# Kernel optimization log

Measured on AMD Instinct MI355X. Metric: run time of the kernel, lower is better.

The kernel has to match this reference:

```python
import jax, jax.numpy as jnp
from jax import lax
import numpy as np

GB_MAX = 3      # BandEst guard-band upper bound
RB = 1          # refer_band
PAD = RB + 1    # refer_band + init_guard_band(1)
N_OFF = 16      # ring offsets: kernel (4,4) -> N=16
BN_EPS = 1e-5

def _ring_offsets():
    idx = np.arange(-PAD, PAD + 1)
    X, Y = np.meshgrid(idx, idx, indexing='ij')
    hp = wp = 2 * PAD + 1
    def ring(M):
        return np.concatenate([M[0:RB, 0:wp - RB].ravel(), M[0:hp - RB, wp - RB:wp].ravel(),
                               M[hp - RB:hp, RB:wp].ravel(), M[RB:hp, 0:RB].ravel()])
    return ring(X).astype(np.float32), ring(Y).astype(np.float32)

PRF_X, PRF_Y = _ring_offsets()
BLOCK = np.repeat(np.arange(4), N_OFF // 4)  # offset n -> direction block (top,right,bottom,left)


def q_shift(x, H, W, shift=1, gamma=0.25):
    B, T, C = x.shape
    img = x.transpose(0, 2, 1).reshape(B, C, H, W)
    g = int(C * gamma)
    out = jnp.zeros_like(img)
    out = out.at[:, 0:g, :, shift:].set(img[:, 0:g, :, :W - shift])
    out = out.at[:, g:2 * g, :, :W - shift].set(img[:, g:2 * g, :, shift:])
    out = out.at[:, 2 * g:3 * g, shift:, :].set(img[:, 2 * g:3 * g, :H - shift, :])
    out = out.at[:, 3 * g:4 * g, :H - shift, :].set(img[:, 3 * g:4 * g, shift:, :])
    out = out.at[:, 4 * g:].set(img[:, 4 * g:])
    return out.reshape(B, C, T).transpose(0, 2, 1)


def bi_wkv(w, u, k, v):
    # Bi-directional WKV: y_t = (sum_{i<t} e^{-(t-1-i)w + k_i} v_i + e^{u+k_t} v_t
    #                            + sum_{i>t} e^{-(i-1-t)w + k_i} v_i) / (same with v->1)
    B, T, C = k.shape
    kT = k.transpose(1, 0, 2)
    vT = v.transpose(1, 0, 2)

    def step(carry, kv):
        m, a, b = carry  # state represents e^m * (a, b): (sum exp, weighted v)
        kt, vt = kv
        out = (m, a, b)  # exclusive prefix (excludes current token)
        m2 = jnp.maximum(m - w, kt)
        e1 = jnp.exp(m - w - m2)
        e2 = jnp.exp(kt - m2)
        return (m2, e1 * a + e2, e1 * b + e2 * vt), out

    init = (jnp.full((B, C), -1e38, k.dtype), jnp.zeros((B, C), k.dtype), jnp.zeros((B, C), k.dtype))
    _, (mf, af, bf) = lax.scan(step, init, (kT, vT))
    _, (mb, ab, bb) = lax.scan(step, init, (kT[::-1], vT[::-1]))
    mb, ab, bb = mb[::-1], ab[::-1], bb[::-1]
    ms = u + kT
    M = jnp.maximum(jnp.maximum(mf, mb), ms)
    ef, eb, es = jnp.exp(mf - M), jnp.exp(mb - M), jnp.exp(ms - M)
    num = ef * bf + eb * bb + es * vT
    den = ef * af + eb * ab + es
    return (num / den).transpose(1, 0, 2)


def band_est(x, cvw, cvb, bns_v, bnb_v, chw, chb, bns_h, bnb_h):
    dn = ('NCHW', 'OIHW', 'NCHW')
    gv = lax.conv_general_dilated(x, cvw, (1, 1), ((GB_MAX, GB_MAX), (0, 0)), dimension_numbers=dn) + cvb[None, :, None, None]
    gh = lax.conv_general_dilated(x, chw, (1, 1), ((0, 0), (GB_MAX, GB_MAX)), dimension_numbers=dn) + chb[None, :, None, None]
    inv = np.float32(1.0 / np.sqrt(1.0 + BN_EPS))  # eval BN: running mean 0, var 1
    gv = gv * (bns_v * inv)[None, :, None, None] + bnb_v[None, :, None, None]
    gh = gh * (bns_h * inv)[None, :, None, None] + bnb_h[None, :, None, None]
    return jnp.concatenate([jax.nn.sigmoid(gv), jax.nn.sigmoid(gh)], 1) * (GB_MAX - 1)


def _gather(xp_flat, ix, iy, wp, h, w):
    b, c = xp_flat.shape[0], xp_flat.shape[1]
    idx = (ix * wp + iy).reshape(b, 1, -1)
    return jnp.take_along_axis(xp_flat, idx, axis=2).reshape(b, c, h, w, N_OFF)


def ada_peak(x_img, cvw, cvb, bns_v, bnb_v, chw, chb, bns_h, bnb_h):
    b, c, h, w = x_img.shape
    xp = jnp.pad(x_img, ((0, 0), (0, 0), (PAD, PAD), (PAD, PAD)), mode='edge')
    hp, wp = h + 2 * PAD, w + 2 * PAD
    xp_flat = xp.reshape(b, c, hp * wp)
    gb = band_est(x_img, cvw, cvb, bns_v, bnb_v, chw, chb, bns_h, bnb_h)  # (b,4,h,w)
    zero = jnp.zeros_like(gb[:, 0])
    mvx = jnp.stack([-gb[:, 0], zero, gb[:, 1], zero], -1)  # (b,h,w,4) per block
    mvy = jnp.stack([zero, gb[:, 3], zero, -gb[:, 2]], -1)
    move_x = mvx[..., BLOCK]  # (b,h,w,16)
    move_y = mvy[..., BLOCK]
    cx = jnp.arange(PAD, h + PAD, dtype=x_img.dtype)
    cy = jnp.arange(PAD, w + PAD, dtype=x_img.dtype)
    px = cx[None, :, None, None] + jnp.asarray(PRF_X)[None, None, None, :] + move_x
    py = cy[None, None, :, None] + jnp.asarray(PRF_Y)[None, None, None, :] + move_y
    flx = jnp.floor(lax.stop_gradient(px))
    fly = jnp.floor(lax.stop_gradient(py))
    q_lt_x = jnp.clip(flx, 0, hp - 1)
    q_lt_y = jnp.clip(fly, 0, wp - 1)
    q_rb_x = jnp.clip(flx + 1, 0, hp - 1)
    q_rb_y = jnp.clip(fly + 1, 0, wp - 1)
    pxc = jnp.clip(px, 0, hp - 1)
    pyc = jnp.clip(py, 0, wp - 1)
    g_lt = (1 + (q_lt_x - pxc)) * (1 + (q_lt_y - pyc))
    g_rb = (1 - (q_rb_x - pxc)) * (1 - (q_rb_y - pyc))
    x_lt = _gather(xp_flat, q_lt_x.astype(jnp.int32), q_lt_y.astype(jnp.int32), wp, h, w)
    x_rb = _gather(xp_flat, q_rb_x.astype(jnp.int32), q_rb_y.astype(jnp.int32), wp, h, w)
    x_r = g_lt[:, None] * x_lt + g_rb[:, None] * x_rb
    return x_img[..., None] - x_r  # (b,c,h,w,N): center-minus-reference peak feature


def setup_inputs():
    key = jax.random.key(0)
    B, H, W, C = 2, 64, 64, 192
    ks = jax.random.split(key, 16)
    s = 0.02
    return {
        'x': jax.random.normal(ks[0], (B, H * W, C), jnp.float32),
        'h': H, 'w': W,
        'mix_k': jax.random.uniform(ks[1], (1, 1, C), jnp.float32),
        'mix_v': jax.random.uniform(ks[2], (1, 1, C), jnp.float32),
        'mix_r': jax.random.uniform(ks[3], (1, 1, C), jnp.float32),
        'Wk': jax.random.normal(ks[4], (C, C), jnp.float32) * s,
        'Wv': jax.random.normal(ks[5], (C, C), jnp.float32) * s,
        'Wr': jax.random.normal(ks[6], (C, C), jnp.float32) * s,
        'Wo': jax.random.normal(ks[7], (C, C), jnp.float32) * s,
        'spatial_decay': jax.random.normal(ks[8], (C,), jnp.float32),
        'spatial_first': jax.random.normal(ks[9], (C,), jnp.float32),
        'cvw': jax.random.normal(ks[10], (2, C, 2 * GB_MAX + 1, 1), jnp.float32) * s,
        'cvb': jnp.zeros((2,), jnp.float32),
        'bns_v': jnp.ones((2,), jnp.float32),
        'bnb_v': jnp.zeros((2,), jnp.float32),
        'chw': jax.random.normal(ks[11], (2, C, 1, 2 * GB_MAX + 1), jnp.float32) * s,
        'chb': jnp.zeros((2,), jnp.float32),
        'bns_h': jnp.ones((2,), jnp.float32),
        'bnb_h': jnp.zeros((2,), jnp.float32),
    }


def reference(x, h, w, mix_k, mix_v, mix_r, Wk, Wv, Wr, Wo, spatial_decay, spatial_first,
              cvw, cvb, bns_v, bnb_v, chw, chb, bns_h, bnb_h):
    B, T, C = x.shape
    xx = q_shift(x, h, w)
    xk = x * mix_k + xx * (1 - mix_k)
    xv = x * mix_v + xx * (1 - mix_v)
    xr = x * mix_r + xx * (1 - mix_r)
    k = xk @ Wk
    v = xv @ Wv
    sr = jax.nn.sigmoid(xr @ Wr)
    # deformable peak branch (AdaPeak2D) on the token grid, pooled over the N=16 ring samples
    x_img = x.transpose(0, 2, 1).reshape(B, C, h, w)
    peak = ada_peak(x_img, cvw, cvb, bns_v, bnb_v, chw, chb, bns_h, bnb_h).mean(-1)
    v = v + peak.reshape(B, C, T).transpose(0, 2, 1)
    y = bi_wkv(spatial_decay / T, spatial_first / T, k, v)
    return (sr * y) @ Wo
```

## Files before the change

### kernel.cpp

```cpp
#include <hip/hip_runtime.h>
#include <hip/hip_bf16.h>

#define BATCH 2
#define TLEN 4096
#define CC 192
#define NTOT 576
#define PADC 2

__device__ __constant__ float PRF_X[16] = {-2,-2,-2,-2, -2,-1,0,1, 2,2,2,2, -1,0,1,2};
__device__ __constant__ float PRF_Y[16] = {-2,-1,0,1, 2,2,2,2, -1,0,1,2, -2,-2,-2,-2};

#define ASWZ(n) ((n) + (((n) >> 5) << 2))

__global__ __launch_bounds__(256) void k_build_wcat(const float* __restrict__ Wk,
                                                    const float* __restrict__ Wv,
                                                    const float* __restrict__ Wr,
                                                    const float* __restrict__ mk,
                                                    const float* __restrict__ mv,
                                                    const float* __restrict__ mr,
                                                    float* __restrict__ Wcat) {
    int idx = blockIdx.x * 256 + threadIdx.x;
    if (idx >= 384 * NTOT) return;
    int r   = idx / NTOT;
    int col = idx - r * NTOT;
    int cb = col / CC;
    int cc = col - cb * CC;
    const float* W   = (cb == 0) ? Wk : (cb == 1) ? Wv : Wr;
    const float* mix = (cb == 0) ? mk : (cb == 1) ? mv : mr;
    float v;
    if (r < CC) v = mix[r] * W[r * CC + cc];
    else        v = (1.0f - mix[r - CC]) * W[(r - CC) * CC + cc];
    Wcat[idx] = v;
}

__global__ __launch_bounds__(256) void k_gemm1(const float* __restrict__ x,
                                               const float* __restrict__ Wcat,
                                               float* __restrict__ ZTk,
                                               float* __restrict__ Zv,
                                               float* __restrict__ ZTr) {
    __shared__ float As[2][16][140];
    __shared__ float Bs[2][16][68];
    const int tid = threadIdx.x;
    const int bm = blockIdx.y * 128;
    const int bn = blockIdx.x * 64;
    const int tx = tid & 15, ty = tid >> 4;
    const int ar  = tid >> 1;
    const int akh = (tid & 1) * 8;
    const int bk  = tid >> 4;
    const int bn4 = (tid & 15) * 4;

    const int row = bm + ar;
    const int t   = row & (TLEN - 1);
    const int ri  = t >> 6, rj = t & 63;

    float acc[8][4] = {};
    float4 a0, a1, b0;

    auto loadG = [&](int k0, float4& ra0, float4& ra1, float4& rb0) {
        if (k0 < CC) {
            const float* pa = x + (size_t)row * CC + k0 + akh;
            ra0 = *(const float4*)pa;
            ra1 = *(const float4*)(pa + 4);
        } else {
            int c = k0 - CC + akh;
            int g = c / 48;
            int dr; bool ok;
            if      (g == 0) { dr = -1;  ok = (rj > 0);  }
            else if (g == 1) { dr =  1;  ok = (rj < 63); }
            else if (g == 2) { dr = -64; ok = (ri > 0);  }
            else             { dr =  64; ok = (ri < 63); }
            if (ok) {
                const float* pa = x + (size_t)(row + dr) * CC + c;
                ra0 = *(const float4*)pa;
                ra1 = *(const float4*)(pa + 4);
            } else {
                ra0 = make_float4(0.f, 0.f, 0.f, 0.f);
                ra1 = make_float4(0.f, 0.f, 0.f, 0.f);
            }
        }
        rb0 = *(const float4*)(Wcat + (size_t)(k0 + bk) * NTOT + bn + bn4);
    };
    auto stage = [&](int buf, float4 ra0, float4 ra1, float4 rb0) {
        int sa = ASWZ(ar);
        As[buf][akh + 0][sa] = ra0.x; As[buf][akh + 1][sa] = ra0.y;
        As[buf][akh + 2][sa] = ra0.z; As[buf][akh + 3][sa] = ra0.w;
        As[buf][akh + 4][sa] = ra1.x; As[buf][akh + 5][sa] = ra1.y;
        As[buf][akh + 6][sa] = ra1.z; As[buf][akh + 7][sa] = ra1.w;
        *(float4*)&Bs[buf][bk][bn4] = rb0;
    };

    loadG(0, a0, a1, b0);
    stage(0, a0, a1, b0);
    __syncthreads();

    const int abase = ASWZ(ty * 8);
    int buf = 0;
    for (int it = 0; it < 24; ++it) {
        if (it < 23) loadG((it + 1) * 16, a0, a1, b0);
#pragma unroll
        for (int kk = 0; kk < 16; ++kk) {
            float av[8], bv[4];
            *(float4*)&av[0] = *(const float4*)&As[buf][kk][abase];
            *(float4*)&av[4] = *(const float4*)&As[buf][kk][abase + 4];
            *(float4*)&bv[0] = *(const float4*)&Bs[buf][kk][tx * 4];
#pragma unroll
            for (int ii = 0; ii < 8; ++ii)
#pragma unroll
                for (int jj = 0; jj < 4; ++jj)
                    acc[ii][jj] = fmaf(av[ii], bv[jj], acc[ii][jj]);
        }
        if (it < 23) {
            stage(buf ^ 1, a0, a1, b0);
            __syncthreads();
            buf ^= 1;
        }
    }

    const int sec = bn / CC;
    const int col0 = bn - sec * CC + tx * 4;
    if (sec == 1) {
#pragma unroll
        for (int ii = 0; ii < 8; ++ii) {
            int r2 = bm + ty * 8 + ii;
            float4 o = {acc[ii][0], acc[ii][1], acc[ii][2], acc[ii][3]};
            *(float4*)(Zv + (size_t)r2 * CC + col0) = o;
        }
    } else {
        float* D = (sec == 0) ? ZTk : ZTr;
        int row0 = bm + ty * 8;
#pragma unroll
        for (int jj = 0; jj < 4; ++jj) {
            float4 o0 = {acc[0][jj], acc[1][jj], acc[2][jj], acc[3][jj]};
            float4 o1 = {acc[4][jj], acc[5][jj], acc[6][jj], acc[7][jj]};
            float* p = D + (size_t)(col0 + jj) * 8192 + row0;
            *(float4*)p = o0;
            *(float4*)(p + 4) = o1;
        }
    }
}

__global__ __launch_bounds__(256) void k_gemm2(const float* __restrict__ AT,
                                               const float* __restrict__ B,
                                               float* __restrict__ Cmat) {
    __shared__ float As[2][16][132];
    __shared__ float Bs[2][16][68];
    const int tid = threadIdx.x;
    const int bm = blockIdx.y * 128;
    const int bn = blockIdx.x * 64;
    const int tx = tid & 15, ty = tid >> 4;
    const int ak  = tid >> 4;
    const int am8 = (tid & 15) * 8;
    const int bkr = tid >> 4;
    const int bn4 = (tid & 15) * 4;

    float acc[8][4] = {};
    float4 a0, a1, b0;

    auto loadG = [&](int k0, float4& ra0, float4& ra1, float4& rb0) {
        const float* pa = AT + (size_t)(k0 + ak) * 8192 + bm + am8;
        ra0 = *(const float4*)pa;
        ra1 = *(const float4*)(pa + 4);
        rb0 = *(const float4*)(B + (size_t)(k0 + bkr) * CC + bn + bn4);
    };
    auto stage = [&](int buf, float4 ra0, float4 ra1, float4 rb0) {
        *(float4*)&As[buf][ak][am8]     = ra0;
        *(float4*)&As[buf][ak][am8 + 4] = ra1;
        *(float4*)&Bs[buf][bkr][bn4]    = rb0;
    };

    loadG(0, a0, a1, b0);
    stage(0, a0, a1, b0);
    __syncthreads();

    int buf = 0;
    for (int it = 0; it < 12; ++it) {
        if (it < 11) loadG((it + 1) * 16, a0, a1, b0);
#pragma unroll
        for (int kk = 0; kk < 16; ++kk) {
            float av[8], bv[4];
            *(float4*)&av[0] = *(const float4*)&As[buf][kk][ty * 8];
            *(float4*)&av[4] = *(const float4*)&As[buf][kk][ty * 8 + 4];
            *(float4*)&bv[0] = *(const float4*)&Bs[buf][kk][tx * 4];
#pragma unroll
            for (int ii = 0; ii < 8; ++ii)
#pragma unroll
                for (int jj = 0; jj < 4; ++jj)
                    acc[ii][jj] = fmaf(av[ii], bv[jj], acc[ii][jj]);
        }
        if (it < 11) {
            stage(buf ^ 1, a0, a1, b0);
            __syncthreads();
            buf ^= 1;
        }
    }
#pragma unroll
    for (int ii = 0; ii < 8; ++ii) {
        int row = bm + ty * 8 + ii;
        float4 o0 = {acc[ii][0], acc[ii][1], acc[ii][2], acc[ii][3]};
        *(float4*)(Cmat + (size_t)row * CC + bn + tx * 4) = o0;
    }
}

__global__ __launch_bounds__(192) void k_bandpeak(const float* __restrict__ x,
                                                  const float* __restrict__ cvw,
                                                  const float* __restrict__ cvb,
                                                  const float* __restrict__ bns_v,
                                                  const float* __restrict__ bnb_v,
                                                  const float* __restrict__ chw,
                                                  const float* __restrict__ chb,
                                                  const float* __restrict__ bns_h,
                                                  const float* __restrict__ bnb_h,
                                                  float* __restrict__ Zv) {
    int pixg = blockIdx.x;
    int b   = pixg >> 12;
    int pix = pixg & 4095;
    int i = pix >> 6, j = pix & 63;
    int c = threadIdx.x;
    size_t xbase = (size_t)b * TLEN * CC;

    float sv0 = 0.f, sv1 = 0.f, sh0 = 0.f, sh1 = 0.f;
#pragma unroll
    for (int t = 0; t < 7; ++t) {
        int ii = i + t - 3;
        if (ii >= 0 && ii < 64) {
            float xv = x[xbase + (size_t)(ii * 64 + j) * CC + c];
            sv0 = fmaf(xv, cvw[(0 * CC + c) * 7 + t], sv0);
            sv1 = fmaf(xv, cvw[(1 * CC + c) * 7 + t], sv1);
        }
        int jj = j + t - 3;
        if (jj >= 0 && jj < 64) {
            float xh = x[xbase + (size_t)(i * 64 + jj) * CC + c];
            sh0 = fmaf(xh, chw[(0 * CC + c) * 7 + t], sh0);
            sh1 = fmaf(xh, chw[(1 * CC + c) * 7 + t], sh1);
        }
    }
    __shared__ float red[4][CC];
    __shared__ float gsh[4];
    red[0][c] = sv0; red[1][c] = sv1; red[2][c] = sh0; red[3][c] = sh1;
    __syncthreads();
    if (c < 64) {
#pragma unroll
        for (int r = 0; r < 4; ++r) {
            float v = red[r][c] + red[r][c + 64] + red[r][c + 128];
            v += __shfl_xor(v, 32);
            v += __shfl_xor(v, 16);
            v += __shfl_xor(v, 8);
            v += __shfl_xor(v, 4);
            v += __shfl_xor(v, 2);
            v += __shfl_xor(v, 1);
            if (c == 0) {
                const float inv = 0.9999950000374997f;
                float bias, sc, sh;
                if (r < 2) { bias = cvb[r];     sc = bns_v[r];     sh = bnb_v[r]; }
                else       { bias = chb[r - 2]; sc = bns_h[r - 2]; sh = bnb_h[r - 2]; }
                float g = (v + bias) * (sc * inv) + sh;
                gsh[r] = 2.0f / (1.0f + expf(-g));
            }
        }
    }
    __syncthreads();

    __shared__ int   l_lt[16], l_rb[16];
    __shared__ float l_glt[16], l_grb[16];
    if (c < 16) {
        int n = c, blk = n >> 2;
        float mx = (blk == 0) ? -gsh[0] : (blk == 2) ? gsh[1] : 0.0f;
        float my = (blk == 1) ?  gsh[3] : (blk == 3) ? -gsh[2] : 0.0f;
        float px = (float)(i + PADC) + PRF_X[n] + mx;
        float py = (float)(j + PADC) + PRF_Y[n] + my;
        float flx = floorf(px), fly = floorf(py);
        float qltx = fminf(fmaxf(flx, 0.f), 67.f);
        float qlty = fminf(fmaxf(fly, 0.f), 67.f);
        float qrbx = fminf(fmaxf(flx + 1.f, 0.f), 67.f);
        float qrby = fminf(fmaxf(fly + 1.f, 0.f), 67.f);
        float pxc = fminf(fmaxf(px, 0.f), 67.f);
        float pyc = fminf(fmaxf(py, 0.f), 67.f);
        float glt = (1.f + (qltx - pxc)) * (1.f + (qlty - pyc));
        float grb = (1.f - (qrbx - pxc)) * (1.f - (qrby - pyc));
        int sltx = min(max((int)qltx - PADC, 0), 63);
        int slty = min(max((int)qlty - PADC, 0), 63);
        int srbx = min(max((int)qrbx - PADC, 0), 63);
        int srby = min(max((int)qrby - PADC, 0), 63);
        l_lt[n] = sltx * 64 + slty;
        l_rb[n] = srbx * 64 + srby;
        l_glt[n] = glt;
        l_grb[n] = grb;
    }
    __syncthreads();

    float acc = 0.f;
#pragma unroll
    for (int n = 0; n < 16; ++n) {
        acc = fmaf(l_glt[n], x[xbase + (size_t)l_lt[n] * CC + c], acc);
        acc = fmaf(l_grb[n], x[xbase + (size_t)l_rb[n] * CC + c], acc);
    }
    float peak = x[xbase + (size_t)pix * CC + c] - acc * 0.0625f;
    Zv[((size_t)b * TLEN + pix) * CC + c] += peak;
}

__global__ __launch_bounds__(256) void k_transv(const float* __restrict__ Zv,
                                                float* __restrict__ ZTv) {
    __shared__ float tile[64][65];
    int tid = threadIdx.x;
    int rb = (blockIdx.x & 127) * 64;
    int cb = (blockIdx.x >> 7) * 64;
    int tr  = tid >> 4;
    int tc4 = (tid & 15) * 4;
#pragma unroll
    for (int q = 0; q < 4; ++q) {
        int r = tr + q * 16;
        float4 v = *(const float4*)(Zv + (size_t)(rb + r) * CC + cb + tc4);
        *(float4*)&tile[r][tc4] = v;
    }
    __syncthreads();
#pragma unroll
    for (int q = 0; q < 4; ++q) {
        int ccol = tr + q * 16;
        float4 o = {tile[tc4 + 0][ccol], tile[tc4 + 1][ccol],
                    tile[tc4 + 2][ccol], tile[tc4 + 3][ccol]};
        *(float4*)(ZTv + (size_t)(cb + ccol) * 8192 + rb + tc4) = o;
    }
}

__global__ __launch_bounds__(256) void k_wkv2(const float* __restrict__ ZT,
                                              float* __restrict__ PT,
                                              const float* __restrict__ sd,
                                              const float* __restrict__ sf) {
    const int NTH = 256, CH = 16;
    int c = blockIdx.x % CC;
    int b = blockIdx.x / CC;
    const float w = sd[c] * (1.0f / 4096.0f);
    const float u = sf[c] * (1.0f / 4096.0f);

    __shared__ float s_m[NTH], s_a[NTH], s_b[NTH], s_L[NTH];

    int tid = threadIdx.x;
    int s = tid * CH;
    size_t rowbase = (size_t)b * TLEN;

    float kr[CH], vr[CH], rr[CH];
    {
        const float* pk = ZT + (size_t)c * 8192 + rowbase + s;
        const float* pv = ZT + (size_t)(CC + c) * 8192 + rowbase + s;
        const float* pr = ZT + (size_t)(2 * CC + c) * 8192 + rowbase + s;
#pragma unroll
        for (int q = 0; q < 4; ++q) {
            *(float4*)&kr[q * 4] = *(const float4*)(pk + q * 4);
            *(float4*)&vr[q * 4] = *(const float4*)(pv + q * 4);
            *(float4*)&rr[q * 4] = *(const float4*)(pr + q * 4);
        }
    }

    float m = -1e38f, a = 0.f, bb = 0.f;
#pragma unroll
    for (int jj = 0; jj < CH; ++jj) {
        float kt = kr[jj], vt = vr[jj];
        float m2 = fmaxf(m - w, kt);
        float e1 = expf(m - w - m2);
        float e2 = expf(kt - m2);
        a = e1 * a + e2;
        bb = e1 * bb + e2 * vt;
        m = m2;
    }
    s_m[tid] = m; s_a[tid] = a; s_b[tid] = bb; s_L[tid] = (float)CH;
    float L = (float)CH;
    for (int d = 1; d < NTH; d <<= 1) {
        __syncthreads();
        float pm = 0, pa = 0, pb = 0, pL = 0;
        bool has = (tid >= d);
        if (has) { pm = s_m[tid - d]; pa = s_a[tid - d]; pb = s_b[tid - d]; pL = s_L[tid - d]; }
        __syncthreads();
        if (has) {
            float pdec = pm - L * w;
            float m2 = fmaxf(pdec, m);
            float e1 = expf(pdec - m2);
            float e2 = expf(m - m2);
            a  = e1 * pa + e2 * a;
            bb = e1 * pb + e2 * bb;
            m = m2; L += pL;
            s_m[tid] = m; s_a[tid] = a; s_b[tid] = bb; s_L[tid] = L;
        }
    }
    __syncthreads();
    float fm = -1e38f, fa = 0.f, fb = 0.f;
    if (tid > 0) { fm = s_m[tid - 1]; fa = s_a[tid - 1]; fb = s_b[tid - 1]; }
    __syncthreads();

    m = -1e38f; a = 0.f; bb = 0.f;
#pragma unroll
    for (int jj = CH - 1; jj >= 0; --jj) {
        float kt = kr[jj], vt = vr[jj];
        float m2 = fmaxf(m - w, kt);
        float e1 = expf(m - w - m2);
        float e2 = expf(kt - m2);
        a = e1 * a + e2;
        bb = e1 * bb + e2 * vt;
        m = m2;
    }
    s_m[tid] = m; s_a[tid] = a; s_b[tid] = bb; s_L[tid] = (float)CH;
    L = (float)CH;
    for (int d = 1; d < NTH; d <<= 1) {
        __syncthreads();
        float pm = 0, pa = 0, pb = 0, pL = 0;
        bool has = (tid + d) < NTH;
        if (has) { pm = s_m[tid + d]; pa = s_a[tid + d]; pb = s_b[tid + d]; pL = s_L[tid + d]; }
        __syncthreads();
        if (has) {
            float pdec = pm - L * w;
            float m2 = fmaxf(m, pdec);
            float e1 = expf(m - m2);
            float e2 = expf(pdec - m2);
            a  = e1 * a + e2 * pa;
            bb = e1 * bb + e2 * pb;
            m = m2; L += pL;
            s_m[tid] = m; s_a[tid] = a; s_b[tid] = bb; s_L[tid] = L;
        }
    }
    __syncthreads();
    float bm = -1e38f, ba = 0.f, bbv = 0.f;
    if (tid < NTH - 1) { bm = s_m[tid + 1]; ba = s_a[tid + 1]; bbv = s_b[tid + 1]; }

    float em[CH], ea[CH], eb[CH];
    m = bm; a = ba; bb = bbv;
#pragma unroll
    for (int jj = CH - 1; jj >= 0; --jj) {
        em[jj] = m; ea[jj] = a; eb[jj] = bb;
        float kt = kr[jj], vt = vr[jj];
        float m2 = fmaxf(m - w, kt);
        float e1 = expf(m - w - m2);
        float e2 = expf(kt - m2);
        a = e1 * a + e2;
        bb = e1 * bb + e2 * vt;
        m = m2;
    }

    m = fm; a = fa; bb = fb;
#pragma unroll
    for (int jj = 0; jj < CH; ++jj) {
        float kt = kr[jj], vt = vr[jj];
        float ms = u + kt;
        float M = fmaxf(fmaxf(m, em[jj]), ms);
        float ef  = expf(m - M);
        float ebk = expf(em[jj] - M);
        float es  = expf(ms - M);
        float num = ef * bb + ebk * eb[jj] + es * vt;
        float den = ef * a + ebk * ea[jj] + es;
        float y = num / den;
        float sr = 1.0f / (1.0f + expf(-rr[jj]));
        PT[(size_t)c * 8192 + rowbase + s + jj] = sr * y;
        float m2 = fmaxf(m - w, kt);
        float e1 = expf(m - w - m2);
        float e2 = expf(kt - m2);
        a = e1 * a + e2;
        bb = e1 * bb + e2 * vt;
        m = m2;
    }
}

extern "C" void kernel_launch(void* const* d_in, const int* in_sizes, int n_in,
                              void* d_out, int out_size, void* d_ws, size_t ws_size,
                              hipStream_t stream) {
    const float* x     = (const float*)d_in[0];
    const float* mix_k = (const float*)d_in[3];
    const float* mix_v = (const float*)d_in[4];
    const float* mix_r = (const float*)d_in[5];
    const float* Wk    = (const float*)d_in[6];
    const float* Wv    = (const float*)d_in[7];
    const float* Wr    = (const float*)d_in[8];
    const float* Wo    = (const float*)d_in[9];
    const float* sd    = (const float*)d_in[10];
    const float* sf    = (const float*)d_in[11];
    const float* cvw   = (const float*)d_in[12];
    const float* cvb   = (const float*)d_in[13];
    const float* bns_v = (const float*)d_in[14];
    const float* bnb_v = (const float*)d_in[15];
    const float* chw   = (const float*)d_in[16];
    const float* chb   = (const float*)d_in[17];
    const float* bns_h = (const float*)d_in[18];
    const float* bnb_h = (const float*)d_in[19];
    float* out = (float*)d_out;
    float* ws  = (float*)d_ws;

    float* Zv   = ws;
    float* ZT   = ws + 1572864;
    float* Wcat = ws + 6291456;
    float* ZTk  = ZT;
    float* ZTv  = ZT + 1572864;
    float* ZTr  = ZT + 3145728;
    float* PT   = Zv;

    k_build_wcat<<<864, 256, 0, stream>>>(Wk, Wv, Wr, mix_k, mix_v, mix_r, Wcat);
    k_gemm1<<<dim3(9, 64), 256, 0, stream>>>(x, Wcat, ZTk, Zv, ZTr);
    k_bandpeak<<<8192, 192, 0, stream>>>(x, cvw, cvb, bns_v, bnb_v, chw, chb, bns_h, bnb_h, Zv);
    k_transv<<<384, 256, 0, stream>>>(Zv, ZTv);
    k_wkv2<<<384, 256, 0, stream>>>(ZT, PT, sd, sf);
    k_gemm2<<<dim3(3, 64), 256, 0, stream>>>(PT, Wo, out);
}
```

Measured before the change: 238.4 us.

## Run both projection GEMMs on bf16 MFMA with split hi/lo precision

Replaces the FP32 FMA tiled GEMMs with MFMA bf16 kernels. Each fp32 operand is split into a high and a low bf16 part, and three MFMA products are summed to keep near-fp32 accuracy. New prep kernels split x, build the transposed mixed weight and Wo matrices, and transpose/split the WKV output into row-major bf16. This adds extra passes and memory traffic for the conversions in exchange for much higher matrix throughput.

```diff
diff --git a/kernel.cpp b/kernel.cpp
--- a/kernel.cpp
+++ b/kernel.cpp
@@ -4,200 +4,289 @@
 #define BATCH 2
 #define TLEN 4096
 #define CC 192
-#define NTOT 576
 #define PADC 2
+
+typedef __attribute__((ext_vector_type(8))) short bf16x8;
+typedef __attribute__((ext_vector_type(4))) float f32x4;
 
 __device__ __constant__ float PRF_X[16] = {-2,-2,-2,-2, -2,-1,0,1, 2,2,2,2, -1,0,1,2};
 __device__ __constant__ float PRF_Y[16] = {-2,-1,0,1, 2,2,2,2, -1,0,1,2, -2,-2,-2,-2};
 
-#define ASWZ(n) ((n) + (((n) >> 5) << 2))
-
-__global__ __launch_bounds__(256) void k_build_wcat(const float* __restrict__ Wk,
-                                                    const float* __restrict__ Wv,
-                                                    const float* __restrict__ Wr,
-                                                    const float* __restrict__ mk,
-                                                    const float* __restrict__ mv,
-                                                    const float* __restrict__ mr,
-                                                    float* __restrict__ Wcat) {
+__device__ __forceinline__ unsigned short f2bf(float f) {
+    unsigned u = __float_as_uint(f);
+    u = (u + 0x7FFF + ((u >> 16) & 1)) >> 16;
+    return (unsigned short)u;
+}
+__device__ __forceinline__ float bf2f(unsigned short h) {
+    return __uint_as_float(((unsigned)h) << 16);
+}
+
+__global__ __launch_bounds__(256) void k_split_x(const float* __restrict__ x,
+                                                 unsigned short* __restrict__ XH,
+                                                 unsigned short* __restrict__ XL,
+                                                 unsigned short* __restrict__ ZP) {
+    if (blockIdx.x == 0 && threadIdx.x < 32) ZP[threadIdx.x] = 0;
     int idx = blockIdx.x * 256 + threadIdx.x;
-    if (idx >= 384 * NTOT) return;
-    int r   = idx / NTOT;
-    int col = idx - r * NTOT;
-    int cb = col / CC;
-    int cc = col - cb * CC;
-    const float* W   = (cb == 0) ? Wk : (cb == 1) ? Wv : Wr;
-    const float* mix = (cb == 0) ? mk : (cb == 1) ? mv : mr;
-    float v;
-    if (r < CC) v = mix[r] * W[r * CC + cc];
-    else        v = (1.0f - mix[r - CC]) * W[(r - CC) * CC + cc];
-    Wcat[idx] = v;
-}
-
-__global__ __launch_bounds__(256) void k_gemm1(const float* __restrict__ x,
-                                               const float* __restrict__ Wcat,
-                                               float* __restrict__ ZTk,
-                                               float* __restrict__ Zv,
-                                               float* __restrict__ ZTr) {
-    __shared__ float As[2][16][140];
-    __shared__ float Bs[2][16][68];
-    const int tid = threadIdx.x;
+    float4 v = *(const float4*)(x + (size_t)idx * 4);
+    ushort4 hh, ll;
+    float f, fh;
+    f = v.x; hh.x = f2bf(f); fh = bf2f(hh.x); ll.x = f2bf(f - fh);
+    f = v.y; hh.y = f2bf(f); fh = bf2f(hh.y); ll.y = f2bf(f - fh);
+    f = v.z; hh.z = f2bf(f); fh = bf2f(hh.z); ll.z = f2bf(f - fh);
+    f = v.w; hh.w = f2bf(f); fh = bf2f(hh.w); ll.w = f2bf(f - fh);
+    *(ushort4*)(XH + (size_t)idx * 4) = hh;
+    *(ushort4*)(XL + (size_t)idx * 4) = ll;
+}
+
+__global__ __launch_bounds__(256) void k_wcat_t(const float* __restrict__ Wk,
+                                                const float* __restrict__ Wv,
+                                                const float* __restrict__ Wr,
+                                                const float* __restrict__ mk,
+                                                const float* __restrict__ mv,
+                                                const float* __restrict__ mr,
+                                                unsigned short* __restrict__ WTH,
+                                                unsigned short* __restrict__ WTL) {
+    int idx = blockIdx.x * 256 + threadIdx.x;
+    int n = idx / 384, k = idx - n * 384;
+    int sec = n / CC, nc = n - sec * CC;
+    const float* W   = (sec == 0) ? Wk : (sec == 1) ? Wv : Wr;
+    const float* mix = (sec == 0) ? mk : (sec == 1) ? mv : mr;
+    float wv = (k < CC) ? mix[k] * W[k * CC + nc]
+                        : (1.0f - mix[k - CC]) * W[(k - CC) * CC + nc];
+    unsigned short h = f2bf(wv);
+    WTH[idx] = h;
+    WTL[idx] = f2bf(wv - bf2f(h));
+}
+
+__global__ __launch_bounds__(256) void k_prep_wo(const float* __restrict__ Wo,
+                                                 unsigned short* __restrict__ WoTH,
+                                                 unsigned short* __restrict__ WoTL) {
+    int idx = blockIdx.x * 256 + threadIdx.x;
+    int n = idx / CC, k = idx - n * CC;
+    float wv = Wo[k * CC + n];
+    unsigned short h = f2bf(wv);
+    WoTH[idx] = h;
+    WoTL[idx] = f2bf(wv - bf2f(h));
+}
+
+__global__ __launch_bounds__(128, 2) void k_gemm1_mfma(
+        const unsigned short* __restrict__ XH, const unsigned short* __restrict__ XL,
+        const unsigned short* __restrict__ WTH, const unsigned short* __restrict__ WTL,
+        const unsigned short* __restrict__ ZP,
+        float* __restrict__ ZTk, float* __restrict__ Zv, float* __restrict__ ZTr) {
+    __shared__ unsigned short sAh[128 * 32], sAl[128 * 32];
+    __shared__ unsigned short sBh[64 * 32],  sBl[64 * 32];
+    const int tid  = threadIdx.x;
+    const int w    = tid >> 6;
+    const int lane = tid & 63;
+    const int bx = blockIdx.x;
     const int bm = blockIdx.y * 128;
+    const int bn = bx * 64;
+
+    const int lc  = tid & 3;
+    const int ar0 = tid >> 2;
+
+    f32x4 acc[4][4];
+#pragma unroll
+    for (int i = 0; i < 4; ++i)
+#pragma unroll
+        for (int j = 0; j < 4; ++j) acc[i][j] = f32x4{0.f, 0.f, 0.f, 0.f};
+
+    uint4 rA[8], rB[4];
+
+    auto loadA = [&](int step) {
+        int k0 = step * 32;
+#pragma unroll
+        for (int q = 0; q < 4; ++q) {
+            int rloc = ar0 + q * 32;
+            int rg = bm + rloc;
+            const unsigned short *srcH, *srcL;
+            if (k0 < CC) {
+                size_t o = (size_t)rg * CC + k0 + lc * 8;
+                srcH = XH + o; srcL = XL + o;
+            } else {
+                int c = k0 - CC + lc * 8;
+                int g = c / 48;
+                int t = rg & (TLEN - 1);
+                int ri = t >> 6, rj = t & 63;
+                int dr; bool ok;
+                if      (g == 0) { dr = -1;  ok = (rj > 0);  }
+                else if (g == 1) { dr =  1;  ok = (rj < 63); }
+                else if (g == 2) { dr = -64; ok = (ri > 0);  }
+                else             { dr =  64; ok = (ri < 63); }
+                if (ok) { size_t o = (size_t)(rg + dr) * CC + c; srcH = XH + o; srcL = XL + o; }
+                else    { srcH = ZP; srcL = ZP; }
+            }
+            rA[q * 2]     = *(const uint4*)srcH;
+            rA[q * 2 + 1] = *(const uint4*)srcL;
+        }
+    };
+    auto loadB = [&](int step) {
+        int k0 = step * 32;
+#pragma unroll
+        for (int q = 0; q < 2; ++q) {
+            int col = ar0 + q * 32;
+            size_t o = (size_t)(bn + col) * 384 + k0 + lc * 8;
+            rB[q * 2]     = *(const uint4*)(WTH + o);
+            rB[q * 2 + 1] = *(const uint4*)(WTL + o);
+        }
+    };
+    auto writeS = [&]() {
+#pragma unroll
+        for (int q = 0; q < 4; ++q) {
+            int off = (ar0 + q * 32) * 32 + lc * 8;
+            *(uint4*)&sAh[off] = rA[q * 2];
+            *(uint4*)&sAl[off] = rA[q * 2 + 1];
+        }
+#pragma unroll
+        for (int q = 0; q < 2; ++q) {
+            int off = (ar0 + q * 32) * 32 + lc * 8;
+            *(uint4*)&sBh[off] = rB[q * 2];
+            *(uint4*)&sBl[off] = rB[q * 2 + 1];
+        }
+    };
+
+    const int r15 = lane & 15, ksub = lane >> 4;
+    const int pc8 = ksub * 8;
+
+    loadA(0); loadB(0);
+    for (int step = 0; step < 12; ++step) {
+        __syncthreads();
+        writeS();
+        __syncthreads();
+        if (step < 11) { loadA(step + 1); loadB(step + 1); }
+        bf16x8 ah[4], al[4], bh[4], bl[4];
+#pragma unroll
+        for (int f = 0; f < 4; ++f) {
+            int ra = (w * 64 + f * 16 + r15) * 32 + pc8;
+            ah[f] = *(const bf16x8*)&sAh[ra];
+            al[f] = *(const bf16x8*)&sAl[ra];
+            int rb = (f * 16 + r15) * 32 + pc8;
+            bh[f] = *(const bf16x8*)&sBh[rb];
+            bl[f] = *(const bf16x8*)&sBl[rb];
+        }
+#pragma unroll
+        for (int fr = 0; fr < 4; ++fr)
+#pragma unroll
+            for (int fc = 0; fc < 4; ++fc) {
+                acc[fr][fc] = __builtin_amdgcn_mfma_f32_16x16x32_bf16(ah[fr], bh[fc], acc[fr][fc], 0, 0, 0);
+                acc[fr][fc] = __builtin_amdgcn_mfma_f32_16x16x32_bf16(ah[fr], bl[fc], acc[fr][fc], 0, 0, 0);
+                acc[fr][fc] = __builtin_amdgcn_mfma_f32_16x16x32_bf16(al[fr], bh[fc], acc[fr][fc], 0, 0, 0);
+            }
+    }
+
+    const int sec   = bx / 3;
+    const int cbase = (bx - sec * 3) * 64;
+#pragma unroll
+    for (int fr = 0; fr < 4; ++fr) {
+        int row0 = bm + w * 64 + fr * 16 + ksub * 4;
+#pragma unroll
+        for (int fc = 0; fc < 4; ++fc) {
+            int col = cbase + fc * 16 + r15;
+            f32x4 v = acc[fr][fc];
+            if (sec == 1) {
+#pragma unroll
+                for (int rg = 0; rg < 4; ++rg)
+                    Zv[(size_t)(row0 + rg) * CC + col] = v[rg];
+            } else {
+                float* D = (sec == 0) ? ZTk : ZTr;
+                *(float4*)(D + (size_t)col * 8192 + row0) = make_float4(v[0], v[1], v[2], v[3]);
+            }
+        }
+    }
+}
+
+__global__ __launch_bounds__(128, 2) void k_gemm2_mfma(
+        const unsigned short* __restrict__ PH, const unsigned short* __restrict__ PL,
+        const unsigned short* __restrict__ WoTH, const unsigned short* __restrict__ WoTL,
+        float* __restrict__ out) {
+    __shared__ unsigned short sAh[128 * 32], sAl[128 * 32];
+    __shared__ unsigned short sBh[64 * 32],  sBl[64 * 32];
+    const int tid  = threadIdx.x;
+    const int w    = tid >> 6;
+    const int lane = tid & 63;
     const int bn = blockIdx.x * 64;
-    const int tx = tid & 15, ty = tid >> 4;
-    const int ar  = tid >> 1;
-    const int akh = (tid & 1) * 8;
-    const int bk  = tid >> 4;
-    const int bn4 = (tid & 15) * 4;
-
-    const int row = bm + ar;
-    const int t   = row & (TLEN - 1);
-    const int ri  = t >> 6, rj = t & 63;
-
-    float acc[8][4] = {};
-    float4 a0, a1, b0;
-
-    auto loadG = [&](int k0, float4& ra0, float4& ra1, float4& rb0) {
-        if (k0 < CC) {
-            const float* pa = x + (size_t)row * CC + k0 + akh;
-            ra0 = *(const float4*)pa;
-            ra1 = *(const float4*)(pa + 4);
-        } else {
-            int c = k0 - CC + akh;
-            int g = c / 48;
-            int dr; bool ok;
-            if      (g == 0) { dr = -1;  ok = (rj > 0);  }
-            else if (g == 1) { dr =  1;  ok = (rj < 63); }
-            else if (g == 2) { dr = -64; ok = (ri > 0);  }
-            else             { dr =  64; ok = (ri < 63); }
-            if (ok) {
-                const float* pa = x + (size_t)(row + dr) * CC + c;
-                ra0 = *(const float4*)pa;
-                ra1 = *(const float4*)(pa + 4);
-            } else {
-                ra0 = make_float4(0.f, 0.f, 0.f, 0.f);
-                ra1 = make_float4(0.f, 0.f, 0.f, 0.f);
+    const int bm = blockIdx.y * 128;
+    const int lc  = tid & 3;
+    const int ar0 = tid >> 2;
+
+    f32x4 acc[4][4];
+#pragma unroll
+    for (int i = 0; i < 4; ++i)
+#pragma unroll
+        for (int j = 0; j < 4; ++j) acc[i][j] = f32x4{0.f, 0.f, 0.f, 0.f};
+
+    uint4 rA[8], rB[4];
+    auto loadAB = [&](int step) {
+        int k0 = step * 32;
+#pragma unroll
+        for (int q = 0; q < 4; ++q) {
+            size_t o = (size_t)(bm + ar0 + q * 32) * CC + k0 + lc * 8;
+            rA[q * 2]     = *(const uint4*)(PH + o);
+            rA[q * 2 + 1] = *(const uint4*)(PL + o);
+        }
+#pragma unroll
+        for (int q = 0; q < 2; ++q) {
+            size_t o = (size_t)(bn + ar0 + q * 32) * CC + k0 + lc * 8;
+            rB[q * 2]     = *(const uint4*)(WoTH + o);
+            rB[q * 2 + 1] = *(const uint4*)(WoTL + o);
+        }
+    };
+    auto writeS = [&]() {
+#pragma unroll
+        for (int q = 0; q < 4; ++q) {
+            int off = (ar0 + q * 32) * 32 + lc * 8;
+            *(uint4*)&sAh[off] = rA[q * 2];
+            *(uint4*)&sAl[off] = rA[q * 2 + 1];
+        }
+#pragma unroll
+        for (int q = 0; q < 2; ++q) {
+            int off = (ar0 + q * 32) * 32 + lc * 8;
+            *(uint4*)&sBh[off] = rB[q * 2];
+            *(uint4*)&sBl[off] = rB[q * 2 + 1];
+        }
+    };
+
+    const int r15 = lane & 15, ksub = lane >> 4;
+    const int pc8 = ksub * 8;
+
+    loadAB(0);
+    for (int step = 0; step < 6; ++step) {
+        __syncthreads();
+        writeS();
+        __syncthreads();
+        if (step < 5) loadAB(step + 1);
+        bf16x8 ah[4], al[4], bh[4], bl[4];
+#pragma unroll
+        for (int f = 0; f < 4; ++f) {
+            int ra = (w * 64 + f * 16 + r15) * 32 + pc8;
+            ah[f] = *(const bf16x8*)&sAh[ra];
+            al[f] = *(const bf16x8*)&sAl[ra];
+            int rb = (f * 16 + r15) * 32 + pc8;
+            bh[f] = *(const bf16x8*)&sBh[rb];
+            bl[f] = *(const bf16x8*)&sBl[rb];
+        }
+#pragma unroll
+        for (int fr = 0; fr < 4; ++fr)
+#pragma unroll
+            for (int fc = 0; fc < 4; ++fc) {
+                acc[fr][fc] = __builtin_amdgcn_mfma_f32_16x16x32_bf16(ah[fr], bh[fc], acc[fr][fc], 0, 0, 0);
+                acc[fr][fc] = __builtin_amdgcn_mfma_f32_16x16x32_bf16(ah[fr], bl[fc], acc[fr][fc], 0, 0, 0);
+                acc[fr][fc] = __builtin_amdgcn_mfma_f32_16x16x32_bf16(al[fr], bh[fc], acc[fr][fc], 0, 0, 0);
             }
-        }
-        rb0 = *(const float4*)(Wcat + (size_t)(k0 + bk) * NTOT + bn + bn4);
-    };
-    auto stage = [&](int buf, float4 ra0, float4 ra1, float4 rb0) {
-        int sa = ASWZ(ar);
-        As[buf][akh + 0][sa] = ra0.x; As[buf][akh + 1][sa] = ra0.y;
-        As[buf][akh + 2][sa] = ra0.z; As[buf][akh + 3][sa] = ra0.w;
-        As[buf][akh + 4][sa] = ra1.x; As[buf][akh + 5][sa] = ra1.y;
-        As[buf][akh + 6][sa] = ra1.z; As[buf][akh + 7][sa] = ra1.w;
-        *(float4*)&Bs[buf][bk][bn4] = rb0;
-    };
-
-    loadG(0, a0, a1, b0);
-    stage(0, a0, a1, b0);
-    __syncthreads();
-
-    const int abase = ASWZ(ty * 8);
-    int buf = 0;
-    for (int it = 0; it < 24; ++it) {
-        if (it < 23) loadG((it + 1) * 16, a0, a1, b0);
-#pragma unroll
-        for (int kk = 0; kk < 16; ++kk) {
-            float av[8], bv[4];
-            *(float4*)&av[0] = *(const float4*)&As[buf][kk][abase];
-            *(float4*)&av[4] = *(const float4*)&As[buf][kk][abase + 4];
-            *(float4*)&bv[0] = *(const float4*)&Bs[buf][kk][tx * 4];
-#pragma unroll
-            for (int ii = 0; ii < 8; ++ii)
-#pragma unroll
-                for (int jj = 0; jj < 4; ++jj)
-                    acc[ii][jj] = fmaf(av[ii], bv[jj], acc[ii][jj]);
-        }
-        if (it < 23) {
-            stage(buf ^ 1, a0, a1, b0);
-            __syncthreads();
-            buf ^= 1;
-        }
-    }
-
-    const int sec = bn / CC;
-    const int col0 = bn - sec * CC + tx * 4;
-    if (sec == 1) {
-#pragma unroll
-        for (int ii = 0; ii < 8; ++ii) {
-            int r2 = bm + ty * 8 + ii;
-            float4 o = {acc[ii][0], acc[ii][1], acc[ii][2], acc[ii][3]};
-            *(float4*)(Zv + (size_t)r2 * CC + col0) = o;
-        }
-    } else {
-        float* D = (sec == 0) ? ZTk : ZTr;
-        int row0 = bm + ty * 8;
-#pragma unroll
-        for (int jj = 0; jj < 4; ++jj) {
-            float4 o0 = {acc[0][jj], acc[1][jj], acc[2][jj], acc[3][jj]};
-            float4 o1 = {acc[4][jj], acc[5][jj], acc[6][jj], acc[7][jj]};
-            float* p = D + (size_t)(col0 + jj) * 8192 + row0;
-            *(float4*)p = o0;
-            *(float4*)(p + 4) = o1;
-        }
-    }
-}
-
-__global__ __launch_bounds__(256) void k_gemm2(const float* __restrict__ AT,
-                                               const float* __restrict__ B,
-                                               float* __restrict__ Cmat) {
-    __shared__ float As[2][16][132];
-    __shared__ float Bs[2][16][68];
-    const int tid = threadIdx.x;
-    const int bm = blockIdx.y * 128;
-    const int bn = blockIdx.x * 64;
-    const int tx = tid & 15, ty = tid >> 4;
-    const int ak  = tid >> 4;
-    const int am8 = (tid & 15) * 8;
-    const int bkr = tid >> 4;
-    const int bn4 = (tid & 15) * 4;
-
-    float acc[8][4] = {};
-    float4 a0, a1, b0;
-
-    auto loadG = [&](int k0, float4& ra0, float4& ra1, float4& rb0) {
-        const float* pa = AT + (size_t)(k0 + ak) * 8192 + bm + am8;
-        ra0 = *(const float4*)pa;
-        ra1 = *(const float4*)(pa + 4);
-        rb0 = *(const float4*)(B + (size_t)(k0 + bkr) * CC + bn + bn4);
-    };
-    auto stage = [&](int buf, float4 ra0, float4 ra1, float4 rb0) {
-        *(float4*)&As[buf][ak][am8]     = ra0;
-        *(float4*)&As[buf][ak][am8 + 4] = ra1;
-        *(float4*)&Bs[buf][bkr][bn4]    = rb0;
-    };
-
-    loadG(0, a0, a1, b0);
-    stage(0, a0, a1, b0);
-    __syncthreads();
-
-    int buf = 0;
-    for (int it = 0; it < 12; ++it) {
-        if (it < 11) loadG((it + 1) * 16, a0, a1, b0);
-#pragma unroll
-        for (int kk = 0; kk < 16; ++kk) {
-            float av[8], bv[4];
-            *(float4*)&av[0] = *(const float4*)&As[buf][kk][ty * 8];
-            *(float4*)&av[4] = *(const float4*)&As[buf][kk][ty * 8 + 4];
-            *(float4*)&bv[0] = *(const float4*)&Bs[buf][kk][tx * 4];
-#pragma unroll
-            for (int ii = 0; ii < 8; ++ii)
-#pragma unroll
-                for (int jj = 0; jj < 4; ++jj)
-                    acc[ii][jj] = fmaf(av[ii], bv[jj], acc[ii][jj]);
-        }
-        if (it < 11) {
-            stage(buf ^ 1, a0, a1, b0);
-            __syncthreads();
-            buf ^= 1;
-        }
-    }
-#pragma unroll
-    for (int ii = 0; ii < 8; ++ii) {
-        int row = bm + ty * 8 + ii;
-        float4 o0 = {acc[ii][0], acc[ii][1], acc[ii][2], acc[ii][3]};
-        *(float4*)(Cmat + (size_t)row * CC + bn + tx * 4) = o0;
+    }
+
+#pragma unroll
+    for (int fr = 0; fr < 4; ++fr) {
+        int row0 = bm + w * 64 + fr * 16 + ksub * 4;
+#pragma unroll
+        for (int fc = 0; fc < 4; ++fc) {
+            int col = bn + fc * 16 + r15;
+            f32x4 v = acc[fr][fc];
+#pragma unroll
+            for (int rg = 0; rg < 4; ++rg)
+                out[(size_t)(row0 + rg) * CC + col] = v[rg];
+        }
     }
 }
 
@@ -322,6 +411,37 @@
     }
 }
 
+__global__ __launch_bounds__(256) void k_transP(const float* __restrict__ PT,
+                                                unsigned short* __restrict__ PH,
+                                                unsigned short* __restrict__ PL) {
+    __shared__ float tile[64][65];
+    int tid = threadIdx.x;
+    int mb = (blockIdx.x & 127) * 64;
+    int cb = (blockIdx.x >> 7) * 64;
+    int tr  = tid >> 4;
+    int tc4 = (tid & 15) * 4;
+#pragma unroll
+    for (int q = 0; q < 4; ++q) {
+        int cr = tr + q * 16;
+        float4 v = *(const float4*)(PT + (size_t)(cb + cr) * 8192 + mb + tc4);
+        *(float4*)&tile[cr][tc4] = v;
+    }
+    __syncthreads();
+#pragma unroll
+    for (int q = 0; q < 4; ++q) {
+        int m = tr + q * 16;
+        ushort4 hh, ll;
+        float f, fh;
+        f = tile[tc4 + 0][m]; hh.x = f2bf(f); fh = bf2f(hh.x); ll.x = f2bf(f - fh);
+        f = tile[tc4 + 1][m]; hh.y = f2bf(f); fh = bf2f(hh.y); ll.y = f2bf(f - fh);
+        f = tile[tc4 + 2][m]; hh.z = f2bf(f); fh = bf2f(hh.z); ll.z = f2bf(f - fh);
+        f = tile[tc4 + 3][m]; hh.w = f2bf(f); fh = bf2f(hh.w); ll.w = f2bf(f - fh);
+        size_t o = (size_t)(mb + m) * CC + cb + tc4;
+        *(ushort4*)(PH + o) = hh;
+        *(ushort4*)(PL + o) = ll;
+    }
+}
+
 __global__ __launch_bounds__(256) void k_wkv2(const float* __restrict__ ZT,
                                               float* __restrict__ PT,
                                               const float* __restrict__ sd,
@@ -479,20 +599,30 @@
     const float* bns_h = (const float*)d_in[18];
     const float* bnb_h = (const float*)d_in[19];
     float* out = (float*)d_out;
-    float* ws  = (float*)d_ws;
-
-    float* Zv   = ws;
-    float* ZT   = ws + 1572864;
-    float* Wcat = ws + 6291456;
-    float* ZTk  = ZT;
-    float* ZTv  = ZT + 1572864;
-    float* ZTr  = ZT + 3145728;
-    float* PT   = Zv;
-
-    k_build_wcat<<<864, 256, 0, stream>>>(Wk, Wv, Wr, mix_k, mix_v, mix_r, Wcat);
-    k_gemm1<<<dim3(9, 64), 256, 0, stream>>>(x, Wcat, ZTk, Zv, ZTr);
+    char* W = (char*)d_ws;
+
+    float*          Zv   = (float*)(W + 0);
+    float*          ZTk  = (float*)(W + 6291456);
+    float*          ZTv  = (float*)(W + 12582912);
+    float*          ZTr  = (float*)(W + 18874368);
+    unsigned short* XH   = (unsigned short*)(W + 12582912);
+    unsigned short* XL   = (unsigned short*)(W + 15728640);
+    unsigned short* PH   = (unsigned short*)(W + 6291456);
+    unsigned short* PL   = (unsigned short*)(W + 9437184);
+    float*          PT   = Zv;
+    unsigned short* WTH  = (unsigned short*)(W + 25165824);
+    unsigned short* WTL  = (unsigned short*)(W + 25608192);
+    unsigned short* WoTH = (unsigned short*)(W + 26050560);
+    unsigned short* WoTL = (unsigned short*)(W + 26124288);
+    unsigned short* ZP   = (unsigned short*)(W + 26198016);
+
+    k_split_x<<<1536, 256, 0, stream>>>(x, XH, XL, ZP);
+    k_wcat_t<<<864, 256, 0, stream>>>(Wk, Wv, Wr, mix_k, mix_v, mix_r, WTH, WTL);
+    k_prep_wo<<<144, 256, 0, stream>>>(Wo, WoTH, WoTL);
+    k_gemm1_mfma<<<dim3(9, 64), 128, 0, stream>>>(XH, XL, WTH, WTL, ZP, ZTk, Zv, ZTr);
     k_bandpeak<<<8192, 192, 0, stream>>>(x, cvw, cvb, bns_v, bnb_v, chw, chb, bns_h, bnb_h, Zv);
     k_transv<<<384, 256, 0, stream>>>(Zv, ZTv);
-    k_wkv2<<<384, 256, 0, stream>>>(ZT, PT, sd, sf);
-    k_gemm2<<<dim3(3, 64), 256, 0, stream>>>(PT, Wo, out);
-}
+    k_wkv2<<<384, 256, 0, stream>>>(ZTk, PT, sd, sf);
+    k_transP<<<384, 256, 0, stream>>>(PT, PH, PL);
+    k_gemm2_mfma<<<dim3(3, 64), 128, 0, stream>>>(PH, PL, WoTH, WoTL, out);
+}
```

Measured after the change: 264.4 us. 10.9% more time.
